# Optimization experiments

Hardware: AMD Instinct MI355X
Metric: run time of the kernel (lower is better)

The kernel has to match this reference:

```python
import jax, jax.numpy as jnp
import numpy as np

K = 25          # moving-average kernel_size
P = 24          # periodicity
PAD_LEN = 5     # median padding window (padding_mode='median')


def setup_inputs() -> dict:
    key = jax.random.key(0)
    x = jax.random.normal(key, (64, 128, 8192), dtype=jnp.float32)
    return {"x": x}


def _decompose(x):
    B, C, L = x.shape
    half = (K - 1) // 2  # 12

    # --- moving_average_decomposition with 'median' padding ---
    # torch.median over an odd window (5) == jnp.median
    front = jnp.median(x[:, :, :PAD_LEN], axis=2, keepdims=True)   # [B,C,1]
    end = jnp.median(x[:, :, -PAD_LEN:], axis=2, keepdims=True)    # [B,C,1]
    xp = jnp.concatenate(
        [jnp.repeat(front, half, axis=2), x, jnp.repeat(end, half, axis=2)],
        axis=2,
    )  # [B,C,L+K-1]

    # AvgPool1d(kernel=K, stride=1) via prefix-sum difference (single pass)
    cs = jnp.cumsum(xp, axis=-1)
    cs = jnp.concatenate([jnp.zeros_like(cs[:, :, :1]), cs], axis=-1)
    trend = (cs[:, :, K:] - cs[:, :, :-K]) / K                      # [B,C,L]
    res = x - trend

    # --- per-phase seasonal mean (vectorized replacement of python loop) ---
    pad_len = L % P
    if pad_len > 0:
        # original: cat(res, res[:, :, -P:-pad_len]) -> length divisible by P
        xpad = jnp.concatenate([res, res[:, :, -P:-pad_len]], axis=-1)
    else:
        xpad = res
    n = xpad.shape[-1] // P
    # mean over occurrences of each phase i (== mean of x_padded[:, :, i::P])
    seasonal = jnp.mean(xpad.reshape(B, C, n, P), axis=2)           # [B,C,P]
    out_seasonal = jnp.tile(seasonal, (1, 1, n))[:, :, :L]          # broadcast back
    out_residual = res - out_seasonal
    return out_residual, trend, out_seasonal


def reference(x):
    return _decompose(x)
```

## Files before the change

### kernel.cpp

```cpp
#include <hip/hip_runtime.h>

namespace {
constexpr int LROW   = 8192;
constexpr int KWIN   = 25;
constexpr int HALF   = (KWIN - 1) / 2;
constexpr int PERIOD = 24;
constexpr int NOCC   = 342;
constexpr int NTHR   = 256;
constexpr int GRP    = LROW / (4 * NTHR);
}

__device__ __forceinline__ void ce(float& x, float& y) {
    float lo = fminf(x, y), hi = fmaxf(x, y);
    x = lo; y = hi;
}

__device__ __forceinline__ float median5(float a, float b, float c, float d, float e) {
    ce(a, b); ce(d, e); ce(c, e); ce(c, d); ce(a, d); ce(a, c);
    ce(b, e); ce(b, d); ce(b, c);
    return c;
}

__global__ __launch_bounds__(NTHR, 4) void decomp_kernel(
    const float* __restrict__ x,
    float* __restrict__ out_res,
    float* __restrict__ out_trend,
    float* __restrict__ out_seas)
{
    __shared__ __align__(16) float buf[HALF + LROW + HALF];
    __shared__ float part[240];
    __shared__ float seasonal[PERIOD];
    __shared__ float med_front, med_end;

    float* xs = buf + HALF;
    const int t = threadIdx.x;
    const size_t base = (size_t)blockIdx.x * LROW;
    const float* xr = x + base;

    #pragma unroll
    for (int j = 0; j < GRP; ++j) {
        int g = 4 * (t + NTHR * j);
        *reinterpret_cast<float4*>(xs + g) =
            *reinterpret_cast<const float4*>(xr + g);
    }
    __syncthreads();

    if (t == 0) med_front = median5(xs[0], xs[1], xs[2], xs[3], xs[4]);
    if (t == 1) med_end   = median5(xs[LROW-5], xs[LROW-4], xs[LROW-3],
                                    xs[LROW-2], xs[LROW-1]);
    __syncthreads();

    if (t < HALF)           buf[t] = med_front;
    else if (t < 2 * HALF)  xs[LROW + t - HALF] = med_end;
    __syncthreads();

    float resv[GRP][4];
    #pragma unroll
    for (int j = 0; j < GRP; ++j) {
        int g = 4 * (t + NTHR * j);
        float v[28];
        #pragma unroll
        for (int q = 0; q < 7; ++q) {
            float4 f = *reinterpret_cast<const float4*>(buf + g + 4 * q);
            v[4*q+0] = f.x; v[4*q+1] = f.y; v[4*q+2] = f.z; v[4*q+3] = f.w;
        }
        float s = 0.f;
        #pragma unroll
        for (int q = 0; q < KWIN; ++q) s += v[q];
        constexpr float inv = 1.0f / (float)KWIN;
        float w1 = s  - v[0] + v[25];
        float w2 = w1 - v[1] + v[26];
        float w3 = w2 - v[2] + v[27];
        float t0 = s * inv, t1 = w1 * inv, t2 = w2 * inv, t3 = w3 * inv;
        resv[j][0] = v[12] - t0;
        resv[j][1] = v[13] - t1;
        resv[j][2] = v[14] - t2;
        resv[j][3] = v[15] - t3;
        *reinterpret_cast<float4*>(out_trend + base + g) =
            make_float4(t0, t1, t2, t3);
    }
    __syncthreads();

    #pragma unroll
    for (int j = 0; j < GRP; ++j) {
        int g = 4 * (t + NTHR * j);
        *reinterpret_cast<float4*>(xs + g) =
            make_float4(resv[j][0], resv[j][1], resv[j][2], resv[j][3]);
    }
    __syncthreads();

    if (t < 240) {
        const int p = t / 10, s0 = t % 10;
        float acc = 0.f;
        for (int k = s0; k < NOCC; k += 10) {
            int m = PERIOD * k + p;
            if (m >= LROW) m -= PERIOD;
            acc += xs[m];
        }
        part[t] = acc;
    }
    __syncthreads();
    if (t < PERIOD) {
        float s = 0.f;
        #pragma unroll
        for (int q = 0; q < 10; ++q) s += part[t * 10 + q];
        seasonal[t] = s / (float)NOCC;
    }
    __syncthreads();

    #pragma unroll
    for (int j = 0; j < GRP; ++j) {
        int g = 4 * (t + NTHR * j);
        int ph = g % PERIOD;
        float s0 = seasonal[ph + 0];
        float s1 = seasonal[ph + 1];
        float s2 = seasonal[ph + 2];
        float s3 = seasonal[ph + 3];
        *reinterpret_cast<float4*>(out_seas + base + g) =
            make_float4(s0, s1, s2, s3);
        *reinterpret_cast<float4*>(out_res + base + g) =
            make_float4(resv[j][0] - s0, resv[j][1] - s1,
                        resv[j][2] - s2, resv[j][3] - s3);
    }
}

extern "C" void kernel_launch(void* const* d_in, const int* in_sizes, int n_in,
                              void* d_out, int out_size, void* d_ws, size_t ws_size,
                              hipStream_t stream) {
    const float* x = (const float*)d_in[0];
    float* out = (float*)d_out;
    const size_t n = (size_t)in_sizes[0];
    const int rows = (int)(n / (size_t)LROW);
    decomp_kernel<<<rows, NTHR, 0, stream>>>(x, out, out + n, out + 2 * n);
}
```

Before: 211.0 us.

## Shrink shared memory to one row buffer and handle median padding in registers

```diff
diff --git a/kernel.cpp b/kernel.cpp
--- a/kernel.cpp
+++ b/kernel.cpp
@@ -21,18 +21,14 @@
     return c;
 }
 
-__global__ __launch_bounds__(NTHR, 4) void decomp_kernel(
+__global__ __launch_bounds__(NTHR, 5) void decomp_kernel(
     const float* __restrict__ x,
     float* __restrict__ out_res,
     float* __restrict__ out_trend,
     float* __restrict__ out_seas)
 {
-    __shared__ __align__(16) float buf[HALF + LROW + HALF];
-    __shared__ float part[240];
-    __shared__ float seasonal[PERIOD];
-    __shared__ float med_front, med_end;
+    __shared__ __align__(16) float xs[LROW];
 
-    float* xs = buf + HALF;
     const int t = threadIdx.x;
     const size_t base = (size_t)blockIdx.x * LROW;
     const float* xr = x + base;
@@ -45,24 +41,26 @@
     }
     __syncthreads();
 
-    if (t == 0) med_front = median5(xs[0], xs[1], xs[2], xs[3], xs[4]);
-    if (t == 1) med_end   = median5(xs[LROW-5], xs[LROW-4], xs[LROW-3],
-                                    xs[LROW-2], xs[LROW-1]);
-    __syncthreads();
-
-    if (t < HALF)           buf[t] = med_front;
-    else if (t < 2 * HALF)  xs[LROW + t - HALF] = med_end;
-    __syncthreads();
-
     float resv[GRP][4];
     #pragma unroll
     for (int j = 0; j < GRP; ++j) {
         int g = 4 * (t + NTHR * j);
         float v[28];
-        #pragma unroll
-        for (int q = 0; q < 7; ++q) {
-            float4 f = *reinterpret_cast<const float4*>(buf + g + 4 * q);
-            v[4*q+0] = f.x; v[4*q+1] = f.y; v[4*q+2] = f.z; v[4*q+3] = f.w;
+        if (g >= HALF && g <= LROW - 16) {
+            #pragma unroll
+            for (int q = 0; q < 7; ++q) {
+                float4 f = *reinterpret_cast<const float4*>(xs + g - HALF + 4 * q);
+                v[4*q+0] = f.x; v[4*q+1] = f.y; v[4*q+2] = f.z; v[4*q+3] = f.w;
+            }
+        } else {
+            float med = (g < HALF)
+                ? median5(xs[0], xs[1], xs[2], xs[3], xs[4])
+                : median5(xs[LROW-5], xs[LROW-4], xs[LROW-3], xs[LROW-2], xs[LROW-1]);
+            #pragma unroll
+            for (int q = 0; q < 28; ++q) {
+                int idx = g - HALF + q;
+                v[q] = (idx < 0 || idx >= LROW) ? med : xs[idx];
+            }
         }
         float s = 0.f;
         #pragma unroll
@@ -89,22 +87,23 @@
     }
     __syncthreads();
 
+    float acc = 0.f;
     if (t < 240) {
         const int p = t / 10, s0 = t % 10;
-        float acc = 0.f;
         for (int k = s0; k < NOCC; k += 10) {
             int m = PERIOD * k + p;
             if (m >= LROW) m -= PERIOD;
             acc += xs[m];
         }
-        part[t] = acc;
     }
+    __syncthreads();
+    if (t < 240) xs[t] = acc;
     __syncthreads();
     if (t < PERIOD) {
         float s = 0.f;
         #pragma unroll
-        for (int q = 0; q < 10; ++q) s += part[t * 10 + q];
-        seasonal[t] = s / (float)NOCC;
+        for (int q = 0; q < 10; ++q) s += xs[t * 10 + q];
+        xs[240 + t] = s / (float)NOCC;
     }
     __syncthreads();
 
@@ -112,15 +111,11 @@
     for (int j = 0; j < GRP; ++j) {
         int g = 4 * (t + NTHR * j);
         int ph = g % PERIOD;
-        float s0 = seasonal[ph + 0];
-        float s1 = seasonal[ph + 1];
-        float s2 = seasonal[ph + 2];
-        float s3 = seasonal[ph + 3];
-        *reinterpret_cast<float4*>(out_seas + base + g) =
-            make_float4(s0, s1, s2, s3);
+        float4 sv = *reinterpret_cast<const float4*>(xs + 240 + ph);
+        *reinterpret_cast<float4*>(out_seas + base + g) = sv;
         *reinterpret_cast<float4*>(out_res + base + g) =
-            make_float4(resv[j][0] - s0, resv[j][1] - s1,
-                        resv[j][2] - s2, resv[j][3] - s3);
+            make_float4(resv[j][0] - sv.x, resv[j][1] - sv.y,
+                        resv[j][2] - sv.z, resv[j][3] - sv.w);
     }
 }
 
```

After: 211.3 us, median of 2. No clear change (+0.1%).
